# Optimization experiments

Measured on AMD Instinct MI355X. Metric: run time of the kernel, lower is better.

Reference implementation:

```python
import jax, jax.numpy as jnp
import numpy as np

C_CONST = 8.0   # RG-LRU decay constant (Griffin/Hawk)
EPS = 1e-6      # RMSNorm eps
K = 4           # causal depthwise conv kernel size


def rmsnorm(x, w):
    # x: [B,S,D]
    var = jnp.mean(x * x, axis=-1, keepdims=True)
    return x * jax.lax.rsqrt(var + EPS) * w


def causal_depthwise_conv(x, conv_w, conv_b):
    # x: [B,S,D], conv_w: [K,D], conv_b: [D]; causal (left-pad K-1)
    B, S, D = x.shape
    xp = jnp.pad(x, ((0, 0), (K - 1, 0), (0, 0)))
    out = conv_b
    for k in range(K):  # tiny fixed loop over kernel taps
        out = out + conv_w[k] * xp[:, k:k + S, :]
    return out


def rg_lru(x, Wi, Wa, lam):
    # x: [B,S,D]; diagonal linear recurrence h_t = a_t*h_{t-1} + sqrt(1-a_t^2)*(i_t*x_t)
    r = jax.nn.sigmoid(jnp.einsum('bsd,de->bse', x, Wa))   # recurrence gate
    i = jax.nn.sigmoid(jnp.einsum('bsd,de->bse', x, Wi))   # input gate
    log_a = -C_CONST * jax.nn.softplus(lam) * r            # [B,S,D]
    a = jnp.exp(log_a)
    b = jnp.sqrt(jnp.maximum(1.0 - a * a, 1e-12)) * (i * x)

    def comb(e1, e2):
        a1, b1 = e1
        a2, b2 = e2
        return (a1 * a2, a2 * b1 + b2)

    _, h = jax.lax.associative_scan(comb, (a, b), axis=1)
    return h


def setup_inputs() -> dict:
    key = jax.random.key(0)
    ks = jax.random.split(key, 16)
    B, S, D, H = 4, 2048, 1024, 4096
    s = 0.02
    return {
        'x': jax.random.normal(ks[0], (B, S, D), jnp.float32),
        'norm1_w': jnp.ones((D,), jnp.float32),
        'Wx': jax.random.normal(ks[1], (D, D), jnp.float32) * s,
        'Wy': jax.random.normal(ks[2], (D, D), jnp.float32) * s,
        'conv_w': jax.random.normal(ks[3], (K, D), jnp.float32) * s,
        'conv_b': jnp.zeros((D,), jnp.float32),
        'Wi': jax.random.normal(ks[4], (D, D), jnp.float32) * s,
        'Wa': jax.random.normal(ks[5], (D, D), jnp.float32) * s,
        'lam': jax.random.normal(ks[6], (D,), jnp.float32) * 0.5,
        'Wo': jax.random.normal(ks[7], (D, D), jnp.float32) * s,
        'norm2_w': jnp.ones((D,), jnp.float32),
        'Wg': jax.random.normal(ks[8], (D, H), jnp.float32) * s,
        'Wu': jax.random.normal(ks[9], (D, H), jnp.float32) * s,
        'Wd': jax.random.normal(ks[10], (H, D), jnp.float32) * s,
    }


def reference(x, norm1_w, Wx, Wy, conv_w, conv_b, Wi, Wa, lam, Wo,
              norm2_w, Wg, Wu, Wd):
    # --- mixing block (Hawk recurrent block) with pre-norm + residual ---
    t = rmsnorm(x, norm1_w)
    xb = jnp.einsum('bsd,de->bse', t, Wx)          # recurrence branch
    xb = causal_depthwise_conv(xb, conv_w, conv_b)
    h = rg_lru(xb, Wi, Wa, lam)
    yb = jax.nn.gelu(jnp.einsum('bsd,de->bse', t, Wy))  # gate branch
    mix = jnp.einsum('bsd,de->bse', h * yb, Wo)
    h1 = x + mix
    # --- gated MLP with pre-norm + residual ---
    u = rmsnorm(h1, norm2_w)
    ffn = jnp.einsum('bsh,hd->bsd', jax.nn.gelu(jnp.einsum('bsd,dh->bsh', u, Wg)) * jnp.einsum('bsd,dh->bsh', u, Wu), Wd)
    return h1 + ffn
```

## Files before the change

### kernel.cpp

```cpp
#include <hip/hip_runtime.h>
#include <hip/hip_bf16.h>
#include <stdint.h>

#define B_SZ   4
#define S_LEN  2048
#define D_DIM  1024
#define H_DIM  4096
#define T_TOK  (B_SZ * S_LEN)
#define NC     64
#define CL     32

typedef unsigned short u16;
typedef unsigned int   u32;
typedef __attribute__((ext_vector_type(8))) short short8;
typedef __attribute__((ext_vector_type(4))) float f32x4;

__device__ __forceinline__ float tof(u16 u) {
    union { u32 i; float f; } v; v.i = ((u32)u) << 16; return v.f;
}
__device__ __forceinline__ u16 tobf(float f) {
    union { float f; u32 i; } v; v.f = f;
    u32 x = v.i;
    return (u16)((x + 0x7FFFu + ((x >> 16) & 1u)) >> 16);
}
__device__ __forceinline__ void unp8(uint4 v, float* f) {
    f[0] = tof(v.x & 0xffff); f[1] = tof(v.x >> 16);
    f[2] = tof(v.y & 0xffff); f[3] = tof(v.y >> 16);
    f[4] = tof(v.z & 0xffff); f[5] = tof(v.z >> 16);
    f[6] = tof(v.w & 0xffff); f[7] = tof(v.w >> 16);
}

__device__ __forceinline__ float gelu_f(float x) {
    float x3 = x * x * x;
    float tin = 0.7978845608028654f * (x + 0.044715f * x3);
    float e = __expf(2.f * tin);
    float th = 1.f - 2.f / (e + 1.f);
    return 0.5f * x * (1.f + th);
}
__device__ __forceinline__ float sig_f(float x) {
    return 1.f / (1.f + __expf(-x));
}

__device__ __forceinline__ void gload16(const void* g, void* l) {
    __builtin_amdgcn_global_load_lds(
        (const __attribute__((address_space(1))) u32*)g,
        (__attribute__((address_space(3))) u32*)l,
        16, 0, 0);
}

__global__ void detect_k(const u32* __restrict__ w, int* __restrict__ flag) {
    if (blockIdx.x == 0 && threadIdx.x == 0)
        *flag = (w[0] == 0x3F800000u) ? 1 : 0;
}

__global__ __launch_bounds__(256) void prep_small(
    const void* n1w, const void* n2w, const void* cw, const void* cb,
    const void* lam, u16* n1wc, u16* n2wc, u16* cwc, u16* cbc,
    float* acoef, const int* __restrict__ flagp) {
    int i = blockIdx.x * 256 + threadIdx.x;
    bool f32 = (*flagp) != 0;
    auto rd = [&](const void* p, int j) {
        return f32 ? ((const float*)p)[j] : tof(((const u16*)p)[j]);
    };
    if (i < 1024) n1wc[i] = tobf(rd(n1w, i));
    else if (i < 2048) n2wc[i - 1024] = tobf(rd(n2w, i - 1024));
    else if (i < 6144) cwc[i - 2048] = tobf(rd(cw, i - 2048));
    else if (i < 7168) cbc[i - 6144] = tobf(rd(cb, i - 6144));
    else {
        int d = i - 7168;
        float l = rd(lam, d);
        float sp = fmaxf(l, 0.f) + log1pf(__expf(-fabsf(l)));
        acoef[d] = -8.f * sp;
    }
}

__global__ __launch_bounds__(256) void transpose_any(
    const void* __restrict__ W, u16* __restrict__ WT, int R, int C,
    const int* __restrict__ flag) {
    __shared__ u16 tile[32][33];
    bool f32 = (*flag) != 0;
    int tx = threadIdx.x & 31, ty = threadIdx.x >> 5;
    int c0 = blockIdx.x * 32, r0 = blockIdx.y * 32;
#pragma unroll
    for (int k = 0; k < 4; k++) {
        size_t idx = (size_t)(r0 + ty + k * 8) * C + c0 + tx;
        tile[ty + k * 8][tx] = f32 ? tobf(((const float*)W)[idx])
                                   : ((const u16*)W)[idx];
    }
    __syncthreads();
#pragma unroll
    for (int k = 0; k < 4; k++)
        WT[(size_t)(c0 + ty + k * 8) * R + r0 + tx] = tile[tx][ty + k * 8];
}

__global__ __launch_bounds__(256) void rmsnorm_any(
    const void* __restrict__ X, const u16* __restrict__ Wt, u16* __restrict__ O,
    const int* __restrict__ flagp, int in_mode) {
    bool f32 = in_mode == 1 || (*flagp != 0);
    int row = blockIdx.x;
    int t = threadIdx.x;
    float x0, x1, x2, x3;
    if (f32) {
        float4 v = ((const float4*)((const float*)X + (size_t)row * D_DIM))[t];
        x0 = v.x; x1 = v.y; x2 = v.z; x3 = v.w;
    } else {
        uint2 pv = ((const uint2*)((const u16*)X + (size_t)row * D_DIM))[t];
        x0 = tof(pv.x & 0xffff); x1 = tof(pv.x >> 16);
        x2 = tof(pv.y & 0xffff); x3 = tof(pv.y >> 16);
    }
    float ss = x0 * x0 + x1 * x1 + x2 * x2 + x3 * x3;
#pragma unroll
    for (int off = 32; off; off >>= 1) ss += __shfl_down(ss, off, 64);
    __shared__ float red[4];
    if ((t & 63) == 0) red[t >> 6] = ss;
    __syncthreads();
    float tot = red[0] + red[1] + red[2] + red[3];
    float rs = rsqrtf(tot * (1.f / D_DIM) + 1e-6f);
    uint2 wv = ((const uint2*)Wt)[t];
    float w0 = tof(wv.x & 0xffff), w1 = tof(wv.x >> 16);
    float w2 = tof(wv.y & 0xffff), w3 = tof(wv.y >> 16);
    uint2 ov;
    ov.x = (u32)tobf(x0 * rs * w0) | ((u32)tobf(x1 * rs * w1) << 16);
    ov.y = (u32)tobf(x2 * rs * w2) | ((u32)tobf(x3 * rs * w3) << 16);
    ((uint2*)(O + (size_t)row * D_DIM))[t] = ov;
}

__global__ __launch_bounds__(256) void conv_k(
    const u16* __restrict__ xb, const u16* __restrict__ cw,
    const u16* __restrict__ cb, u16* __restrict__ xc) {
    size_t idx = (size_t)blockIdx.x * 256 + threadIdx.x;
    int dp = (int)(idx & 127);
    size_t ts = idx >> 7;
    int s = (int)(ts & (S_LEN - 1));
    int d0 = dp * 8;
    float acc[8];
    unp8(*(const uint4*)(cb + d0), acc);
    size_t base = ts * D_DIM + d0;
#pragma unroll
    for (int k = 0; k < 4; k++) {
        int sp = s + k - 3;
        if (sp >= 0) {
            float xf[8], wf[8];
            unp8(*(const uint4*)(xb + base + (ptrdiff_t)(k - 3) * D_DIM), xf);
            unp8(*(const uint4*)(cw + k * D_DIM + d0), wf);
#pragma unroll
            for (int e = 0; e < 8; e++) acc[e] += wf[e] * xf[e];
        }
    }
    uint4 ov;
    ov.x = (u32)tobf(acc[0]) | ((u32)tobf(acc[1]) << 16);
    ov.y = (u32)tobf(acc[2]) | ((u32)tobf(acc[3]) << 16);
    ov.z = (u32)tobf(acc[4]) | ((u32)tobf(acc[5]) << 16);
    ov.w = (u32)tobf(acc[6]) | ((u32)tobf(acc[7]) << 16);
    *(uint4*)(xc + base) = ov;
}

__global__ __launch_bounds__(256) void gates_chunk_k(
    const u16* __restrict__ r, const u16* __restrict__ ii, const u16* __restrict__ xc,
    const float* __restrict__ acoef, float2* __restrict__ Ap2, float2* __restrict__ Bs2) {
    int d2 = blockIdx.x * 256 + threadIdx.x;
    int c = blockIdx.y, b = blockIdx.z;
    float ac0 = acoef[d2 * 2], ac1 = acoef[d2 * 2 + 1];
    const u32* r2 = (const u32*)r;
    const u32* i2 = (const u32*)ii;
    const u32* x2 = (const u32*)xc;
    size_t base = ((size_t)b * S_LEN + c * CL) * (D_DIM / 2) + d2;
    float ap0 = 1.f, bs0 = 0.f, ap1 = 1.f, bs1 = 0.f;
    for (int tt = 0; tt < CL; tt++) {
        u32 rv = r2[base], iv = i2[base], xv = x2[base];
        float a0 = __expf(ac0 * tof(rv & 0xffff));
        float a1 = __expf(ac1 * tof(rv >> 16));
        float b0 = sqrtf(fmaxf(1.f - a0 * a0, 1e-12f)) * (tof(iv & 0xffff) * tof(xv & 0xffff));
        float b1 = sqrtf(fmaxf(1.f - a1 * a1, 1e-12f)) * (tof(iv >> 16) * tof(xv >> 16));
        ap0 *= a0; bs0 = fmaf(a0, bs0, b0);
        ap1 *= a1; bs1 = fmaf(a1, bs1, b1);
        base += D_DIM / 2;
    }
    size_t o = ((size_t)b * NC + c) * (D_DIM / 2) + d2;
    Ap2[o] = make_float2(ap0, ap1);
    Bs2[o] = make_float2(bs0, bs1);
}

__global__ __launch_bounds__(256) void carry_k(
    const float2* __restrict__ Ap2, const float2* __restrict__ Bs2,
    float2* __restrict__ carry2) {
    int d2 = blockIdx.x * 256 + threadIdx.x;
    int b = blockIdx.y;
    float2 h = make_float2(0.f, 0.f);
    for (int c = 0; c < NC; c++) {
        size_t o = ((size_t)b * NC + c) * (D_DIM / 2) + d2;
        float2 ap = Ap2[o], bs = Bs2[o];
        carry2[o] = h;
        h.x = fmaf(ap.x, h.x, bs.x);
        h.y = fmaf(ap.y, h.y, bs.y);
    }
}

__global__ __launch_bounds__(256) void apply_k(
    const u16* __restrict__ r, const u16* __restrict__ ii, const u16* __restrict__ xc,
    const float* __restrict__ acoef, const float2* __restrict__ carry2,
    const u16* __restrict__ yb, u16* __restrict__ g) {
    int d2 = blockIdx.x * 256 + threadIdx.x;
    int c = blockIdx.y, b = blockIdx.z;
    float ac0 = acoef[d2 * 2], ac1 = acoef[d2 * 2 + 1];
    float2 h = carry2[((size_t)b * NC + c) * (D_DIM / 2) + d2];
    const u32* r2 = (const u32*)r;
    const u32* i2 = (const u32*)ii;
    const u32* x2 = (const u32*)xc;
    const u32* y2 = (const u32*)yb;
    u32* g2 = (u32*)g;
    size_t base = ((size_t)b * S_LEN + c * CL) * (D_DIM / 2) + d2;
    for (int tt = 0; tt < CL; tt++) {
        u32 rv = r2[base], iv = i2[base], xv = x2[base], yv = y2[base];
        float a0 = __expf(ac0 * tof(rv & 0xffff));
        float a1 = __expf(ac1 * tof(rv >> 16));
        float b0 = sqrtf(fmaxf(1.f - a0 * a0, 1e-12f)) * (tof(iv & 0xffff) * tof(xv & 0xffff));
        float b1 = sqrtf(fmaxf(1.f - a1 * a1, 1e-12f)) * (tof(iv >> 16) * tof(xv >> 16));
        h.x = fmaf(a0, h.x, b0);
        h.y = fmaf(a1, h.y, b1);
        g2[base] = (u32)tobf(h.x * tof(yv & 0xffff)) |
                   ((u32)tobf(h.y * tof(yv >> 16)) << 16);
        base += D_DIM / 2;
    }
}

#define BK 64

enum { EPI_NONE = 0, EPI_GELU = 1, EPI_SIG = 2, EPI_RESID = 3, EPI_MUL = 4 };

template <int E>
__device__ __forceinline__ float epi_apply(float v, const void* aux, size_t idx,
                                           bool auxF32) {
    if (E == EPI_GELU) return gelu_f(v);
    if (E == EPI_SIG) return sig_f(v);
    if (E == EPI_RESID) {
        float a = auxF32 ? ((const float*)aux)[idx] : tof(((const u16*)aux)[idx]);
        return v + a;
    }
    if (E == EPI_MUL) {
        float a = auxF32 ? ((const float*)aux)[idx] : tof(((const u16*)aux)[idx]);
        return v * a;
    }
    return v;
}

template <int BM, int BN, int WMD, int WND, int EPI0, int EPI1, bool OUTF32, bool SWZ>
__global__ __launch_bounds__(WMD * WND * 64, 2) void gemm_db(
    const u16* __restrict__ A, const u16* __restrict__ BT,
    void* __restrict__ C0v, void* __restrict__ C1v, const void* __restrict__ aux,
    const int* __restrict__ flagp, int aux_mode,
    int M, int N, int K, int halfN) {
    constexpr int T  = WMD * WND * 64;
    constexpr int MR = BM / WMD;
    constexpr int NR = BN / WND;
    constexpr int MI = MR / 16;
    constexpr int NJ = NR / 16;
    constexpr int RPR = T / 8;

    __shared__ __align__(16) u16 As[2][BM * BK];
    __shared__ __align__(16) u16 Bs[2][BN * BK];

    const int t = threadIdx.x;
    const int lane = t & 63;
    const int w = t >> 6;
    const int wm = w / WND, wn = w % WND;
    const int quad = lane >> 4, l16 = lane & 15;

    int mt, nt;
    if (SWZ) {
        int GN = gridDim.x;
        int L = blockIdx.y * GN + blockIdx.x;
        int per = (GN * gridDim.y) >> 3;
        int id = (L & 7) * per + (L >> 3);
        mt = id / GN; nt = id - mt * GN;
    } else {
        mt = blockIdx.y; nt = blockIdx.x;
    }
    const int m0 = mt * BM;
    const int n0 = nt * BN;

    const int srow = t >> 3;
    const int cbg  = (t & 7) ^ (srow & 7);
    const u16* ag = A + (size_t)(m0 + srow) * K + cbg * 8;
    const u16* bg = BT + (size_t)(n0 + srow) * K + cbg * 8;
    const size_t rstep = (size_t)RPR * K;

    f32x4 acc[MI][NJ];
#pragma unroll
    for (int i = 0; i < MI; i++)
#pragma unroll
        for (int j = 0; j < NJ; j++) acc[i][j] = (f32x4){0.f, 0.f, 0.f, 0.f};

    const int r7 = l16 & 7;

    auto STAGE = [&](int s, int kt) {
        const u16* a = ag + (size_t)kt * BK;
        const u16* b = bg + (size_t)kt * BK;
        char* lA = (char*)&As[s][0] + t * 16;
        char* lB = (char*)&Bs[s][0] + t * 16;
#pragma unroll
        for (int rr = 0; rr < 4; rr++) {
            gload16(a + rr * rstep, lA + rr * (RPR * 128));
            gload16(b + rr * rstep, lB + rr * (RPR * 128));
        }
    };
    auto COMPUTE = [&](int s) {
#pragma unroll
        for (int kk = 0; kk < 2; kk++) {
            const int cb = ((kk * 4 + quad) ^ r7) * 8;
            short8 af[MI], bf[NJ];
#pragma unroll
            for (int i = 0; i < MI; i++)
                af[i] = *(const short8*)&As[s][(wm * MR + i * 16 + l16) * BK + cb];
#pragma unroll
            for (int j = 0; j < NJ; j++)
                bf[j] = *(const short8*)&Bs[s][(wn * NR + j * 16 + l16) * BK + cb];
#pragma unroll
            for (int i = 0; i < MI; i++)
#pragma unroll
                for (int j = 0; j < NJ; j++)
                    acc[i][j] = __builtin_amdgcn_mfma_f32_16x16x32_bf16(
                        af[i], bf[j], acc[i][j], 0, 0, 0);
        }
    };

    const int NT = K >> 6;
    STAGE(0, 0);
    __syncthreads();
    for (int kt = 0; kt < NT; kt += 2) {
        STAGE(1, kt + 1);
        COMPUTE(0);
        __syncthreads();
        if (kt + 2 < NT) STAGE(0, kt + 2);
        COMPUTE(1);
        __syncthreads();
    }

    const bool auxF32 = (aux_mode == 2) || (aux_mode == 1 && *flagp != 0);
    const int side = (n0 >= halfN) ? 1 : 0;
    void* Cv = side ? C1v : C0v;

#pragma unroll
    for (int i = 0; i < MI; i++) {
        int mbase = m0 + wm * MR + i * 16 + quad * 4;
#pragma unroll
        for (int j = 0; j < NJ; j++) {
            int ncol = n0 - side * halfN + wn * NR + j * 16 + l16;
#pragma unroll
            for (int rr = 0; rr < 4; rr++) {
                size_t idx = (size_t)(mbase + rr) * halfN + ncol;
                float v = acc[i][j][rr];
                v = side ? epi_apply<EPI1>(v, aux, idx, auxF32)
                         : epi_apply<EPI0>(v, aux, idx, auxF32);
                if (OUTF32) ((float*)Cv)[idx] = v;
                else        ((u16*)Cv)[idx] = tobf(v);
            }
        }
    }
}

extern "C" void kernel_launch(void* const* d_in, const int* in_sizes, int n_in,
                              void* d_out, int out_size, void* d_ws, size_t ws_size,
                              hipStream_t stream) {
    const void* x      = d_in[0];
    const void* n1w    = d_in[1];
    const void* Wx     = d_in[2];
    const void* Wy     = d_in[3];
    const void* conv_w = d_in[4];
    const void* conv_b = d_in[5];
    const void* Wi     = d_in[6];
    const void* Wa     = d_in[7];
    const void* lam    = d_in[8];
    const void* Wo     = d_in[9];
    const void* n2w    = d_in[10];
    const void* Wg     = d_in[11];
    const void* Wu     = d_in[12];
    const void* Wd     = d_in[13];
    float* out = (float*)d_out;

    char* ws = (char*)d_ws;
    auto alloc = [&](size_t bytes) {
        char* p = ws;
        ws += (bytes + 255) & ~(size_t)255;
        return p;
    };
    const size_t DD = (size_t)D_DIM * D_DIM;
    const size_t DH = (size_t)D_DIM * H_DIM * 2;
    const size_t TD = (size_t)T_TOK * D_DIM * 2;
    const size_t TH = (size_t)T_TOK * H_DIM * 2;

    int*  dflag  = (int*)alloc(256);
    u16*  n1wc   = (u16*)alloc(D_DIM * 2);
    u16*  n2wc   = (u16*)alloc(D_DIM * 2);
    u16*  cwc    = (u16*)alloc(4 * D_DIM * 2);
    u16*  cbc    = (u16*)alloc(D_DIM * 2);
    float* acoef = (float*)alloc(D_DIM * 4);
    float2* Ap2    = (float2*)alloc((size_t)B_SZ * NC * D_DIM * 4);
    float2* Bs2    = (float2*)alloc((size_t)B_SZ * NC * D_DIM * 4);
    float2* carry2 = (float2*)alloc((size_t)B_SZ * NC * D_DIM * 4);
    u16* WT  = (u16*)alloc(DH);
    u16* T0  = (u16*)alloc(TD);
    u16* T1  = (u16*)alloc(TD);
    u16* T2  = (u16*)alloc(TD);
    u16* T3  = (u16*)alloc(TD);
    u16* T4  = (u16*)alloc(TD);
    u16* ggb = (u16*)alloc(TH);
    float* h1f = (float*)alloc((size_t)T_TOK * D_DIM * 4);

    dim3 b256(256);
    dim3 b512(512);

    detect_k<<<dim3(1), dim3(64), 0, stream>>>((const u32*)n1w, dflag);
    prep_small<<<dim3(32), b256, 0, stream>>>(n1w, n2w, conv_w, conv_b, lam,
                                              n1wc, n2wc, cwc, cbc, acoef, dflag);

    rmsnorm_any<<<dim3(T_TOK), b256, 0, stream>>>(x, n1wc, T2, dflag, 0);

    transpose_any<<<dim3(32, 32), b256, 0, stream>>>(Wx, WT, D_DIM, D_DIM, dflag);
    transpose_any<<<dim3(32, 32), b256, 0, stream>>>(Wy, WT + DD, D_DIM, D_DIM, dflag);
    gemm_db<256, 256, 2, 4, EPI_NONE, EPI_GELU, false, false>
        <<<dim3(2 * D_DIM / 256, T_TOK / 256), b512, 0, stream>>>(
        T2, WT, T1, T3, nullptr, dflag, 0, T_TOK, 2 * D_DIM, D_DIM, D_DIM);

    conv_k<<<dim3(T_TOK * D_DIM / 8 / 256), b256, 0, stream>>>(T1, cwc, cbc, T0);

    transpose_any<<<dim3(32, 32), b256, 0, stream>>>(Wa, WT, D_DIM, D_DIM, dflag);
    transpose_any<<<dim3(32, 32), b256, 0, stream>>>(Wi, WT + DD, D_DIM, D_DIM, dflag);
    gemm_db<256, 256, 2, 4, EPI_SIG, EPI_SIG, false, false>
        <<<dim3(2 * D_DIM / 256, T_TOK / 256), b512, 0, stream>>>(
        T0, WT, T4, T2, nullptr, dflag, 0, T_TOK, 2 * D_DIM, D_DIM, D_DIM);

    gates_chunk_k<<<dim3(2, NC, B_SZ), b256, 0, stream>>>(T4, T2, T0, acoef, Ap2, Bs2);
    carry_k<<<dim3(2, B_SZ), b256, 0, stream>>>(Ap2, Bs2, carry2);
    apply_k<<<dim3(2, NC, B_SZ), b256, 0, stream>>>(T4, T2, T0, acoef, carry2, T3, T4);

    transpose_any<<<dim3(32, 32), b256, 0, stream>>>(Wo, WT, D_DIM, D_DIM, dflag);
    gemm_db<128, 128, 2, 2, EPI_RESID, EPI_RESID, true, false>
        <<<dim3(D_DIM / 128, T_TOK / 128), b256, 0, stream>>>(
        T4, WT, h1f, h1f, x, dflag, 1, T_TOK, D_DIM, D_DIM, D_DIM);

    rmsnorm_any<<<dim3(T_TOK), b256, 0, stream>>>(h1f, n2wc, T1, dflag, 1);

    transpose_any<<<dim3(128, 32), b256, 0, stream>>>(Wg, WT, D_DIM, H_DIM, dflag);
    gemm_db<256, 256, 2, 4, EPI_GELU, EPI_GELU, false, false>
        <<<dim3(H_DIM / 256, T_TOK / 256), b512, 0, stream>>>(
        T1, WT, ggb, ggb, nullptr, dflag, 0, T_TOK, H_DIM, D_DIM, H_DIM);
    transpose_any<<<dim3(128, 32), b256, 0, stream>>>(Wu, WT, D_DIM, H_DIM, dflag);
    gemm_db<256, 256, 2, 4, EPI_MUL, EPI_MUL, false, false>
        <<<dim3(H_DIM / 256, T_TOK / 256), b512, 0, stream>>>(
        T1, WT, ggb, ggb, ggb, dflag, 0, T_TOK, H_DIM, D_DIM, H_DIM);

    transpose_any<<<dim3(32, 128), b256, 0, stream>>>(Wd, WT, H_DIM, D_DIM, dflag);
    gemm_db<128, 128, 2, 2, EPI_RESID, EPI_RESID, true, true>
        <<<dim3(D_DIM / 128, T_TOK / 128), b256, 0, stream>>>(
        ggb, WT, out, out, h1f, dflag, 2, T_TOK, D_DIM, H_DIM, D_DIM);
}
```

Before: 715.5 us.

## Replace double-buffered GEMM with 4-stage BK=32 pipeline and vmcnt-based waits

The GEMM main loop moves from two shared-memory buffers of 64-wide K tiles, with a full __syncthreads after each compute, to four buffers of 32-wide K tiles. Up to three tiles are kept in flight, and each step waits only on the oldest one via s_waitcnt vmcnt plus s_barrier. The LDS swizzle is adapted to the narrower tiles, and s_setprio raises wave priority around the MFMA block. The aim is to hide global-load latency better and cut barrier stalls, at the cost of twice as many loop iterations and barriers per K and hand-tuned wait counts that rely on exactly four loads per stage.

Measured after the change: 747.4 us. 4.5% more time.

```diff
diff --git a/kernel.cpp b/kernel.cpp
--- a/kernel.cpp
+++ b/kernel.cpp
@@ -224,7 +224,6 @@
     }
 }
 
-#define BK 64
 
 enum { EPI_NONE = 0, EPI_GELU = 1, EPI_SIG = 2, EPI_RESID = 3, EPI_MUL = 4 };
 
@@ -245,7 +244,7 @@
 }
 
 template <int BM, int BN, int WMD, int WND, int EPI0, int EPI1, bool OUTF32, bool SWZ>
-__global__ __launch_bounds__(WMD * WND * 64, 2) void gemm_db(
+__global__ __launch_bounds__(WMD * WND * 64, 2) void gemm_p4(
     const u16* __restrict__ A, const u16* __restrict__ BT,
     void* __restrict__ C0v, void* __restrict__ C1v, const void* __restrict__ aux,
     const int* __restrict__ flagp, int aux_mode,
@@ -255,10 +254,12 @@
     constexpr int NR = BN / WND;
     constexpr int MI = MR / 16;
     constexpr int NJ = NR / 16;
-    constexpr int RPR = T / 8;
-
-    __shared__ __align__(16) u16 As[2][BM * BK];
-    __shared__ __align__(16) u16 Bs[2][BN * BK];
+    constexpr int RPR = T / 4;
+    constexpr int AR = BM / RPR;
+    constexpr int BR = BN / RPR;
+
+    __shared__ __align__(16) u16 As[4][BM * 32];
+    __shared__ __align__(16) u16 Bs[4][BN * 32];
 
     const int t = threadIdx.x;
     const int lane = t & 63;
@@ -279,8 +280,8 @@
     const int m0 = mt * BM;
     const int n0 = nt * BN;
 
-    const int srow = t >> 3;
-    const int cbg  = (t & 7) ^ (srow & 7);
+    const int srow = t >> 2;
+    const int cbg  = (t & 3) ^ ((srow >> 1) & 3);
     const u16* ag = A + (size_t)(m0 + srow) * K + cbg * 8;
     const u16* bg = BT + (size_t)(n0 + srow) * K + cbg * 8;
     const size_t rstep = (size_t)RPR * K;
@@ -291,50 +292,53 @@
 #pragma unroll
         for (int j = 0; j < NJ; j++) acc[i][j] = (f32x4){0.f, 0.f, 0.f, 0.f};
 
-    const int r7 = l16 & 7;
+    const int pcb = ((quad ^ ((l16 >> 1) & 3)) * 8);
 
     auto STAGE = [&](int s, int kt) {
-        const u16* a = ag + (size_t)kt * BK;
-        const u16* b = bg + (size_t)kt * BK;
+        const u16* a = ag + (size_t)kt * 32;
+        const u16* b = bg + (size_t)kt * 32;
         char* lA = (char*)&As[s][0] + t * 16;
         char* lB = (char*)&Bs[s][0] + t * 16;
 #pragma unroll
-        for (int rr = 0; rr < 4; rr++) {
-            gload16(a + rr * rstep, lA + rr * (RPR * 128));
-            gload16(b + rr * rstep, lB + rr * (RPR * 128));
-        }
+        for (int rr = 0; rr < AR; rr++)
+            gload16(a + (size_t)rr * rstep, lA + rr * (RPR * 64));
+#pragma unroll
+        for (int rr = 0; rr < BR; rr++)
+            gload16(b + (size_t)rr * rstep, lB + rr * (RPR * 64));
     };
     auto COMPUTE = [&](int s) {
-#pragma unroll
-        for (int kk = 0; kk < 2; kk++) {
-            const int cb = ((kk * 4 + quad) ^ r7) * 8;
-            short8 af[MI], bf[NJ];
-#pragma unroll
-            for (int i = 0; i < MI; i++)
-                af[i] = *(const short8*)&As[s][(wm * MR + i * 16 + l16) * BK + cb];
+        short8 af[MI], bf[NJ];
+#pragma unroll
+        for (int i = 0; i < MI; i++)
+            af[i] = *(const short8*)&As[s][(wm * MR + i * 16 + l16) * 32 + pcb];
+#pragma unroll
+        for (int j = 0; j < NJ; j++)
+            bf[j] = *(const short8*)&Bs[s][(wn * NR + j * 16 + l16) * 32 + pcb];
+        __builtin_amdgcn_s_setprio(1);
+#pragma unroll
+        for (int i = 0; i < MI; i++)
 #pragma unroll
             for (int j = 0; j < NJ; j++)
-                bf[j] = *(const short8*)&Bs[s][(wn * NR + j * 16 + l16) * BK + cb];
-#pragma unroll
-            for (int i = 0; i < MI; i++)
-#pragma unroll
-                for (int j = 0; j < NJ; j++)
-                    acc[i][j] = __builtin_amdgcn_mfma_f32_16x16x32_bf16(
-                        af[i], bf[j], acc[i][j], 0, 0, 0);
-        }
+                acc[i][j] = __builtin_amdgcn_mfma_f32_16x16x32_bf16(
+                    af[i], bf[j], acc[i][j], 0, 0, 0);
+        __builtin_amdgcn_s_setprio(0);
     };
 
-    const int NT = K >> 6;
+    const int NT = K >> 5;
     STAGE(0, 0);
-    __syncthreads();
-    for (int kt = 0; kt < NT; kt += 2) {
-        STAGE(1, kt + 1);
-        COMPUTE(0);
-        __syncthreads();
-        if (kt + 2 < NT) STAGE(0, kt + 2);
-        COMPUTE(1);
-        __syncthreads();
-    }
+    STAGE(1, 1);
+    STAGE(2, 2);
+    int tt = 0;
+    for (; tt < NT - 2; tt++) {
+        asm volatile("s_waitcnt vmcnt(8)\n\ts_barrier" ::: "memory");
+        if (tt + 3 < NT) STAGE((tt + 3) & 3, tt + 3);
+        COMPUTE(tt & 3);
+    }
+    asm volatile("s_waitcnt vmcnt(4)\n\ts_barrier" ::: "memory");
+    COMPUTE(tt & 3);
+    tt++;
+    asm volatile("s_waitcnt vmcnt(0)\n\ts_barrier" ::: "memory");
+    COMPUTE(tt & 3);
 
     const bool auxF32 = (aux_mode == 2) || (aux_mode == 1 && *flagp != 0);
     const int side = (n0 >= halfN) ? 1 : 0;
@@ -418,7 +422,7 @@
 
     transpose_any<<<dim3(32, 32), b256, 0, stream>>>(Wx, WT, D_DIM, D_DIM, dflag);
     transpose_any<<<dim3(32, 32), b256, 0, stream>>>(Wy, WT + DD, D_DIM, D_DIM, dflag);
-    gemm_db<256, 256, 2, 4, EPI_NONE, EPI_GELU, false, false>
+    gemm_p4<256, 256, 2, 4, EPI_NONE, EPI_GELU, false, false>
         <<<dim3(2 * D_DIM / 256, T_TOK / 256), b512, 0, stream>>>(
         T2, WT, T1, T3, nullptr, dflag, 0, T_TOK, 2 * D_DIM, D_DIM, D_DIM);
 
@@ -426,7 +430,7 @@
 
     transpose_any<<<dim3(32, 32), b256, 0, stream>>>(Wa, WT, D_DIM, D_DIM, dflag);
     transpose_any<<<dim3(32, 32), b256, 0, stream>>>(Wi, WT + DD, D_DIM, D_DIM, dflag);
-    gemm_db<256, 256, 2, 4, EPI_SIG, EPI_SIG, false, false>
+    gemm_p4<256, 256, 2, 4, EPI_SIG, EPI_SIG, false, false>
         <<<dim3(2 * D_DIM / 256, T_TOK / 256), b512, 0, stream>>>(
         T0, WT, T4, T2, nullptr, dflag, 0, T_TOK, 2 * D_DIM, D_DIM, D_DIM);
 
@@ -435,23 +439,23 @@
     apply_k<<<dim3(2, NC, B_SZ), b256, 0, stream>>>(T4, T2, T0, acoef, carry2, T3, T4);
 
     transpose_any<<<dim3(32, 32), b256, 0, stream>>>(Wo, WT, D_DIM, D_DIM, dflag);
-    gemm_db<128, 128, 2, 2, EPI_RESID, EPI_RESID, true, false>
+    gemm_p4<128, 128, 2, 2, EPI_RESID, EPI_RESID, true, false>
         <<<dim3(D_DIM / 128, T_TOK / 128), b256, 0, stream>>>(
         T4, WT, h1f, h1f, x, dflag, 1, T_TOK, D_DIM, D_DIM, D_DIM);
 
     rmsnorm_any<<<dim3(T_TOK), b256, 0, stream>>>(h1f, n2wc, T1, dflag, 1);
 
     transpose_any<<<dim3(128, 32), b256, 0, stream>>>(Wg, WT, D_DIM, H_DIM, dflag);
-    gemm_db<256, 256, 2, 4, EPI_GELU, EPI_GELU, false, false>
+    gemm_p4<256, 256, 2, 4, EPI_GELU, EPI_GELU, false, false>
         <<<dim3(H_DIM / 256, T_TOK / 256), b512, 0, stream>>>(
         T1, WT, ggb, ggb, nullptr, dflag, 0, T_TOK, H_DIM, D_DIM, H_DIM);
     transpose_any<<<dim3(128, 32), b256, 0, stream>>>(Wu, WT, D_DIM, H_DIM, dflag);
-    gemm_db<256, 256, 2, 4, EPI_MUL, EPI_MUL, false, false>
+    gemm_p4<256, 256, 2, 4, EPI_MUL, EPI_MUL, false, false>
         <<<dim3(H_DIM / 256, T_TOK / 256), b512, 0, stream>>>(
         T1, WT, ggb, ggb, ggb, dflag, 0, T_TOK, H_DIM, D_DIM, H_DIM);
 
     transpose_any<<<dim3(32, 128), b256, 0, stream>>>(Wd, WT, H_DIM, D_DIM, dflag);
-    gemm_db<128, 128, 2, 2, EPI_RESID, EPI_RESID, true, true>
+    gemm_p4<128, 128, 2, 2, EPI_RESID, EPI_RESID, true, true>
         <<<dim3(D_DIM / 128, T_TOK / 128), b256, 0, stream>>>(
         ggb, WT, out, out, h1f, dflag, 2, T_TOK, D_DIM, H_DIM, D_DIM);
 }
```

## Add 4-stage pipelined 256x256 GEMM with interleaved loads and MFMA halves

Applied to the files above, without the earlier changes.

Introduces a new 256x256 bf16 GEMM kernel that uses a 4-slot shared-memory ring with BK=32 and prefetches two tiles ahead, with XOR-swizzled LDS layout. Each K-step is split into two MFMA halves, with the A and B global loads for the next stages issued between them and s_setprio raised around the MFMA blocks. This kernel replaces the double-buffered gemm_db for the four large 256-tile GEMMs, aiming to hide global-load latency and raise MFMA utilisation. The cost is more barriers per K-step and more reliance on hand-placed waitcnt ordering.

Result: slower. 881.9 us (+23.3%).

```diff
diff --git a/kernel.cpp b/kernel.cpp
--- a/kernel.cpp
+++ b/kernel.cpp
@@ -224,8 +224,6 @@
     }
 }
 
-#define BK 64
-
 enum { EPI_NONE = 0, EPI_GELU = 1, EPI_SIG = 2, EPI_RESID = 3, EPI_MUL = 4 };
 
 template <int E>
@@ -244,6 +242,122 @@
     return v;
 }
 
+template <int EPI0, int EPI1, bool OUTF32>
+__global__ __launch_bounds__(512, 2) void gemm_8p(
+    const u16* __restrict__ A, const u16* __restrict__ BT,
+    void* __restrict__ C0v, void* __restrict__ C1v, const void* __restrict__ aux,
+    const int* __restrict__ flagp, int aux_mode,
+    int M, int N, int K, int halfN) {
+    __shared__ __align__(16) u16 As[4][256 * 32];
+    __shared__ __align__(16) u16 Bs[4][256 * 32];
+
+    const int t = threadIdx.x;
+    const int lane = t & 63;
+    const int w = t >> 6;
+    const int wm = w >> 2, wn = w & 3;
+    const int quad = lane >> 4, l16 = lane & 15;
+
+    const int m0 = blockIdx.y * 256;
+    const int n0 = blockIdx.x * 256;
+
+    const int srow = t >> 2;
+    const int cbg  = (t & 3) ^ ((srow >> 1) & 3);
+    const u16* ag = A + (size_t)(m0 + srow) * K + cbg * 8;
+    const u16* bg = BT + (size_t)(n0 + srow) * K + cbg * 8;
+    const size_t rstep = (size_t)128 * K;
+
+    f32x4 acc[8][4];
+#pragma unroll
+    for (int i = 0; i < 8; i++)
+#pragma unroll
+        for (int j = 0; j < 4; j++) acc[i][j] = (f32x4){0.f, 0.f, 0.f, 0.f};
+
+    const int pcb = (quad ^ ((l16 >> 1) & 3)) * 8;
+
+    auto SA = [&](int s, int kt) {
+        const u16* a = ag + (size_t)kt * 32;
+        char* l = (char*)&As[s][0] + t * 16;
+        gload16(a, l);
+        gload16(a + rstep, l + 8192);
+    };
+    auto SB = [&](int s, int kt) {
+        const u16* b = bg + (size_t)kt * 32;
+        char* l = (char*)&Bs[s][0] + t * 16;
+        gload16(b, l);
+        gload16(b + rstep, l + 8192);
+    };
+
+    const int NT = K >> 5;
+    SA(0, 0); SB(0, 0); SA(1, 1); SB(1, 1);
+    asm volatile("s_waitcnt vmcnt(4)" ::: "memory");
+    __builtin_amdgcn_s_barrier();
+
+    for (int tt = 0; tt < NT; ++tt) {
+        const int s = tt & 3;
+        short8 al[4], ah[4], bfr[4];
+#pragma unroll
+        for (int i = 0; i < 4; i++)
+            al[i] = *(const short8*)&As[s][(wm * 128 + i * 16 + l16) * 32 + pcb];
+#pragma unroll
+        for (int j = 0; j < 4; j++)
+            bfr[j] = *(const short8*)&Bs[s][(wn * 64 + j * 16 + l16) * 32 + pcb];
+        if (tt + 2 < NT) SA((tt + 2) & 3, tt + 2);
+        __builtin_amdgcn_s_barrier();
+        asm volatile("s_waitcnt lgkmcnt(0)" ::: "memory");
+        __builtin_amdgcn_s_setprio(1);
+#pragma unroll
+        for (int i = 0; i < 4; i++)
+#pragma unroll
+            for (int j = 0; j < 4; j++)
+                acc[i][j] = __builtin_amdgcn_mfma_f32_16x16x32_bf16(
+                    al[i], bfr[j], acc[i][j], 0, 0, 0);
+        __builtin_amdgcn_s_setprio(0);
+        __builtin_amdgcn_s_barrier();
+#pragma unroll
+        for (int i = 0; i < 4; i++)
+            ah[i] = *(const short8*)&As[s][(wm * 128 + (i + 4) * 16 + l16) * 32 + pcb];
+        if (tt + 2 < NT) SB((tt + 2) & 3, tt + 2);
+        __builtin_amdgcn_s_barrier();
+        asm volatile("s_waitcnt lgkmcnt(0)" ::: "memory");
+        __builtin_amdgcn_s_setprio(1);
+#pragma unroll
+        for (int i = 0; i < 4; i++)
+#pragma unroll
+            for (int j = 0; j < 4; j++)
+                acc[i + 4][j] = __builtin_amdgcn_mfma_f32_16x16x32_bf16(
+                    ah[i], bfr[j], acc[i + 4][j], 0, 0, 0);
+        __builtin_amdgcn_s_setprio(0);
+        if (tt + 2 < NT)
+            asm volatile("s_waitcnt vmcnt(4)" ::: "memory");
+        else if (tt + 1 < NT)
+            asm volatile("s_waitcnt vmcnt(0)" ::: "memory");
+        __builtin_amdgcn_s_barrier();
+    }
+
+    const bool auxF32 = (aux_mode == 2) || (aux_mode == 1 && *flagp != 0);
+    const int side = (n0 >= halfN) ? 1 : 0;
+    void* Cv = side ? C1v : C0v;
+
+#pragma unroll
+    for (int i = 0; i < 8; i++) {
+        int mbase = m0 + wm * 128 + i * 16 + quad * 4;
+#pragma unroll
+        for (int j = 0; j < 4; j++) {
+            int ncol = n0 - side * halfN + wn * 64 + j * 16 + l16;
+#pragma unroll
+            for (int rr = 0; rr < 4; rr++) {
+                size_t idx = (size_t)(mbase + rr) * halfN + ncol;
+                float v = acc[i][j][rr];
+                v = side ? epi_apply<EPI1>(v, aux, idx, auxF32)
+                         : epi_apply<EPI0>(v, aux, idx, auxF32);
+                if (OUTF32) ((float*)Cv)[idx] = v;
+                else        ((u16*)Cv)[idx] = tobf(v);
+            }
+        }
+    }
+}
+
+#define BK 64
 template <int BM, int BN, int WMD, int WND, int EPI0, int EPI1, bool OUTF32, bool SWZ>
 __global__ __launch_bounds__(WMD * WND * 64, 2) void gemm_db(
     const u16* __restrict__ A, const u16* __restrict__ BT,
@@ -418,7 +532,7 @@
 
     transpose_any<<<dim3(32, 32), b256, 0, stream>>>(Wx, WT, D_DIM, D_DIM, dflag);
     transpose_any<<<dim3(32, 32), b256, 0, stream>>>(Wy, WT + DD, D_DIM, D_DIM, dflag);
-    gemm_db<256, 256, 2, 4, EPI_NONE, EPI_GELU, false, false>
+    gemm_8p<EPI_NONE, EPI_GELU, false>
         <<<dim3(2 * D_DIM / 256, T_TOK / 256), b512, 0, stream>>>(
         T2, WT, T1, T3, nullptr, dflag, 0, T_TOK, 2 * D_DIM, D_DIM, D_DIM);
 
@@ -426,7 +540,7 @@
 
     transpose_any<<<dim3(32, 32), b256, 0, stream>>>(Wa, WT, D_DIM, D_DIM, dflag);
     transpose_any<<<dim3(32, 32), b256, 0, stream>>>(Wi, WT + DD, D_DIM, D_DIM, dflag);
-    gemm_db<256, 256, 2, 4, EPI_SIG, EPI_SIG, false, false>
+    gemm_8p<EPI_SIG, EPI_SIG, false>
         <<<dim3(2 * D_DIM / 256, T_TOK / 256), b512, 0, stream>>>(
         T0, WT, T4, T2, nullptr, dflag, 0, T_TOK, 2 * D_DIM, D_DIM, D_DIM);
 
@@ -442,11 +556,11 @@
     rmsnorm_any<<<dim3(T_TOK), b256, 0, stream>>>(h1f, n2wc, T1, dflag, 1);
 
     transpose_any<<<dim3(128, 32), b256, 0, stream>>>(Wg, WT, D_DIM, H_DIM, dflag);
-    gemm_db<256, 256, 2, 4, EPI_GELU, EPI_GELU, false, false>
+    gemm_8p<EPI_GELU, EPI_GELU, false>
         <<<dim3(H_DIM / 256, T_TOK / 256), b512, 0, stream>>>(
         T1, WT, ggb, ggb, nullptr, dflag, 0, T_TOK, H_DIM, D_DIM, H_DIM);
     transpose_any<<<dim3(128, 32), b256, 0, stream>>>(Wu, WT, D_DIM, H_DIM, dflag);
-    gemm_db<256, 256, 2, 4, EPI_MUL, EPI_MUL, false, false>
+    gemm_8p<EPI_MUL, EPI_MUL, false>
         <<<dim3(H_DIM / 256, T_TOK / 256), b512, 0, stream>>>(
         T1, WT, ggb, ggb, ggb, dflag, 0, T_TOK, H_DIM, D_DIM, H_DIM);
 
```

## Fuse gate and up MLP GEMMs via interleaved weights and GLU epilogue

Applied to the files above, without the earlier changes.

Interleaves the transposed Wg and Wu columns so a single GEMM produces adjacent gate/up pairs. The epilogue combines each pair with a lane shuffle, computing gelu(g)*u and writing one bf16 value. This removes the separate GEMM pass that wrote and re-read the full gelu intermediate, and the second read of the normalized activations. It also enables the swizzled block ordering on all the other GEMMs. The trade-offs are a larger weight workspace and half the lanes idling on stores in the fused epilogue.

Measured after the change: 815.9 us. 14.0% more time.

```diff
diff --git a/kernel.cpp b/kernel.cpp
--- a/kernel.cpp
+++ b/kernel.cpp
@@ -91,6 +91,26 @@
 #pragma unroll
     for (int k = 0; k < 4; k++)
         WT[(size_t)(c0 + ty + k * 8) * R + r0 + tx] = tile[tx][ty + k * 8];
+}
+
+__global__ __launch_bounds__(256) void transpose_ilv(
+    const void* __restrict__ W, u16* __restrict__ WT, int R, int C, int par,
+    const int* __restrict__ flag) {
+    __shared__ u16 tile[32][33];
+    bool f32 = (*flag) != 0;
+    int tx = threadIdx.x & 31, ty = threadIdx.x >> 5;
+    int c0 = blockIdx.x * 32, r0 = blockIdx.y * 32;
+#pragma unroll
+    for (int k = 0; k < 4; k++) {
+        size_t idx = (size_t)(r0 + ty + k * 8) * C + c0 + tx;
+        tile[ty + k * 8][tx] = f32 ? tobf(((const float*)W)[idx])
+                                   : ((const u16*)W)[idx];
+    }
+    __syncthreads();
+#pragma unroll
+    for (int k = 0; k < 4; k++)
+        WT[(size_t)(2 * (c0 + ty + k * 8) + par) * R + r0 + tx] =
+            tile[tx][ty + k * 8];
 }
 
 __global__ __launch_bounds__(256) void rmsnorm_any(
@@ -224,8 +244,6 @@
     }
 }
 
-#define BK 64
-
 enum { EPI_NONE = 0, EPI_GELU = 1, EPI_SIG = 2, EPI_RESID = 3, EPI_MUL = 4 };
 
 template <int E>
@@ -244,7 +262,10 @@
     return v;
 }
 
-template <int BM, int BN, int WMD, int WND, int EPI0, int EPI1, bool OUTF32, bool SWZ>
+#define BK 64
+
+template <int BM, int BN, int WMD, int WND, int EPI0, int EPI1, bool OUTF32,
+          bool SWZ, bool GLU>
 __global__ __launch_bounds__(WMD * WND * 64, 2) void gemm_db(
     const u16* __restrict__ A, const u16* __restrict__ BT,
     void* __restrict__ C0v, void* __restrict__ C1v, const void* __restrict__ aux,
@@ -337,7 +358,7 @@
     }
 
     const bool auxF32 = (aux_mode == 2) || (aux_mode == 1 && *flagp != 0);
-    const int side = (n0 >= halfN) ? 1 : 0;
+    const int side = (!GLU && n0 >= halfN) ? 1 : 0;
     void* Cv = side ? C1v : C0v;
 
 #pragma unroll
@@ -348,12 +369,23 @@
             int ncol = n0 - side * halfN + wn * NR + j * 16 + l16;
 #pragma unroll
             for (int rr = 0; rr < 4; rr++) {
-                size_t idx = (size_t)(mbase + rr) * halfN + ncol;
                 float v = acc[i][j][rr];
-                v = side ? epi_apply<EPI1>(v, aux, idx, auxF32)
-                         : epi_apply<EPI0>(v, aux, idx, auxF32);
-                if (OUTF32) ((float*)Cv)[idx] = v;
-                else        ((u16*)Cv)[idx] = tobf(v);
+                if (GLU) {
+                    float o = __shfl_xor(v, 1);
+                    bool odd = (l16 & 1) != 0;
+                    float gg = odd ? o : v;
+                    float uu = odd ? v : o;
+                    float res = gelu_f(gg) * uu;
+                    if (!odd)
+                        ((u16*)C0v)[(size_t)(mbase + rr) * halfN + (ncol >> 1)]
+                            = tobf(res);
+                } else {
+                    size_t idx = (size_t)(mbase + rr) * halfN + ncol;
+                    v = side ? epi_apply<EPI1>(v, aux, idx, auxF32)
+                             : epi_apply<EPI0>(v, aux, idx, auxF32);
+                    if (OUTF32) ((float*)Cv)[idx] = v;
+                    else        ((u16*)Cv)[idx] = tobf(v);
+                }
             }
         }
     }
@@ -398,7 +430,7 @@
     float2* Ap2    = (float2*)alloc((size_t)B_SZ * NC * D_DIM * 4);
     float2* Bs2    = (float2*)alloc((size_t)B_SZ * NC * D_DIM * 4);
     float2* carry2 = (float2*)alloc((size_t)B_SZ * NC * D_DIM * 4);
-    u16* WT  = (u16*)alloc(DH);
+    u16* WT  = (u16*)alloc(2 * DH);
     u16* T0  = (u16*)alloc(TD);
     u16* T1  = (u16*)alloc(TD);
     u16* T2  = (u16*)alloc(TD);
@@ -418,7 +450,7 @@
 
     transpose_any<<<dim3(32, 32), b256, 0, stream>>>(Wx, WT, D_DIM, D_DIM, dflag);
     transpose_any<<<dim3(32, 32), b256, 0, stream>>>(Wy, WT + DD, D_DIM, D_DIM, dflag);
-    gemm_db<256, 256, 2, 4, EPI_NONE, EPI_GELU, false, false>
+    gemm_db<256, 256, 2, 4, EPI_NONE, EPI_GELU, false, true, false>
         <<<dim3(2 * D_DIM / 256, T_TOK / 256), b512, 0, stream>>>(
         T2, WT, T1, T3, nullptr, dflag, 0, T_TOK, 2 * D_DIM, D_DIM, D_DIM);
 
@@ -426,7 +458,7 @@
 
     transpose_any<<<dim3(32, 32), b256, 0, stream>>>(Wa, WT, D_DIM, D_DIM, dflag);
     transpose_any<<<dim3(32, 32), b256, 0, stream>>>(Wi, WT + DD, D_DIM, D_DIM, dflag);
-    gemm_db<256, 256, 2, 4, EPI_SIG, EPI_SIG, false, false>
+    gemm_db<256, 256, 2, 4, EPI_SIG, EPI_SIG, false, true, false>
         <<<dim3(2 * D_DIM / 256, T_TOK / 256), b512, 0, stream>>>(
         T0, WT, T4, T2, nullptr, dflag, 0, T_TOK, 2 * D_DIM, D_DIM, D_DIM);
 
@@ -435,23 +467,22 @@
     apply_k<<<dim3(2, NC, B_SZ), b256, 0, stream>>>(T4, T2, T0, acoef, carry2, T3, T4);
 
     transpose_any<<<dim3(32, 32), b256, 0, stream>>>(Wo, WT, D_DIM, D_DIM, dflag);
-    gemm_db<128, 128, 2, 2, EPI_RESID, EPI_RESID, true, false>
+    gemm_db<128, 128, 2, 2, EPI_RESID, EPI_RESID, true, true, false>
         <<<dim3(D_DIM / 128, T_TOK / 128), b256, 0, stream>>>(
         T4, WT, h1f, h1f, x, dflag, 1, T_TOK, D_DIM, D_DIM, D_DIM);
 
     rmsnorm_any<<<dim3(T_TOK), b256, 0, stream>>>(h1f, n2wc, T1, dflag, 1);
 
-    transpose_any<<<dim3(128, 32), b256, 0, stream>>>(Wg, WT, D_DIM, H_DIM, dflag);
-    gemm_db<256, 256, 2, 4, EPI_GELU, EPI_GELU, false, false>
-        <<<dim3(H_DIM / 256, T_TOK / 256), b512, 0, stream>>>(
-        T1, WT, ggb, ggb, nullptr, dflag, 0, T_TOK, H_DIM, D_DIM, H_DIM);
-    transpose_any<<<dim3(128, 32), b256, 0, stream>>>(Wu, WT, D_DIM, H_DIM, dflag);
-    gemm_db<256, 256, 2, 4, EPI_MUL, EPI_MUL, false, false>
-        <<<dim3(H_DIM / 256, T_TOK / 256), b512, 0, stream>>>(
-        T1, WT, ggb, ggb, ggb, dflag, 0, T_TOK, H_DIM, D_DIM, H_DIM);
+    transpose_ilv<<<dim3(H_DIM / 32, D_DIM / 32), b256, 0, stream>>>(
+        Wg, WT, D_DIM, H_DIM, 0, dflag);
+    transpose_ilv<<<dim3(H_DIM / 32, D_DIM / 32), b256, 0, stream>>>(
+        Wu, WT, D_DIM, H_DIM, 1, dflag);
+    gemm_db<256, 256, 2, 4, EPI_NONE, EPI_NONE, false, true, true>
+        <<<dim3(2 * H_DIM / 256, T_TOK / 256), b512, 0, stream>>>(
+        T1, WT, ggb, ggb, nullptr, dflag, 0, T_TOK, 2 * H_DIM, D_DIM, H_DIM);
 
     transpose_any<<<dim3(32, 128), b256, 0, stream>>>(Wd, WT, H_DIM, D_DIM, dflag);
-    gemm_db<128, 128, 2, 2, EPI_RESID, EPI_RESID, true, true>
+    gemm_db<128, 128, 2, 2, EPI_RESID, EPI_RESID, true, true, false>
         <<<dim3(D_DIM / 128, T_TOK / 128), b256, 0, stream>>>(
         ggb, WT, out, out, h1f, dflag, 2, T_TOK, D_DIM, H_DIM, D_DIM);
 }
```
